# Optimization experiments

Hardware: AMD Instinct MI355X
Metric: run time of the kernel (lower is better)

The kernel has to match this reference:

```python
import jax, jax.numpy as jnp
import numpy as np
from jax import lax

B, C, H, W = 16, 128, 128, 128
WS, K = 2, 7
EPS = 1e-5


def setup_inputs() -> dict:
    key = jax.random.key(0)
    ks = jax.random.split(key, 4)
    s = 0.02
    return {
        "x": jax.random.normal(ks[0], (B, C, H, W), jnp.float32),
        "bn_gamma": jnp.ones((C,), jnp.float32),
        "bn_beta": jnp.zeros((C,), jnp.float32),
        "bn_mean": jnp.zeros((C,), jnp.float32),
        "bn_var": jnp.ones((C,), jnp.float32),
        "dw_w": jax.random.normal(ks[1], (C, 1, K, K), jnp.float32) * s,  # depthwise OIHW, groups=C
        "dw_b": jnp.zeros((C,), jnp.float32),
        "qkv_w": jax.random.normal(ks[2], (3 * C, C), jnp.float32) * s,  # 1x1 conv weight
        "qkv_b": jnp.zeros((3 * C,), jnp.float32),
        "proj_w": jax.random.normal(ks[3], (C, C), jnp.float32) * s,
        "proj_b": jnp.zeros((C,), jnp.float32),
    }


def reference(x, bn_gamma, bn_beta, bn_mean, bn_var, dw_w, dw_b, qkv_w, qkv_b, proj_w, proj_b):
    b, c, h, w = x.shape
    h2, w2 = h // WS, w // WS
    L = h2 * w2
    # --- ggm: BatchNorm (eval) -> GELU -> depthwise conv k=7 stride=2 pad=3 ---
    inv = lax.rsqrt(bn_var + EPS)
    xn = (x - bn_mean[None, :, None, None]) * (bn_gamma * inv)[None, :, None, None] + bn_beta[None, :, None, None]
    g = jax.nn.gelu(xn, approximate=False)
    guide = lax.conv_general_dilated(
        g, dw_w, window_strides=(WS, WS), padding=[(K // 2, K // 2), (K // 2, K // 2)],
        feature_group_count=c, dimension_numbers=("NCHW", "OIHW", "NCHW"),
    ) + dw_b[None, :, None, None]  # [B,C,H2,W2]
    # --- unfold(kernel=2, stride=2): non-overlapping 2x2 windows -> [B,C,4,L] ---
    xu = x.reshape(b, c, h2, WS, w2, WS).transpose(0, 1, 3, 5, 2, 4).reshape(b, c, WS * WS, L)
    tokens = jnp.concatenate([guide.reshape(b, c, 1, L), xu], axis=2)  # [B,C,5,L]
    # --- qkv 1x1 conv ---
    qkv = jnp.einsum("bcnl,dc->bdnl", tokens, qkv_w) + qkv_b[None, :, None, None]
    q, k, v = jnp.split(qkv, 3, axis=1)  # each [B,C,5,L]
    # --- tiny 5x5 attention per channel, contracting over the L window axis ---
    attn = jnp.einsum("bcnl,bcml->bcnm", q, k) / jnp.sqrt(jnp.float32(c))
    attn = jax.nn.softmax(attn, axis=-1)
    out = jnp.einsum("bcnm,bcml->bcnl", attn, v)  # [B,C,5,L]
    # take the guide-token row and fold back to the window grid
    out0 = out[:, :, 0, :].reshape(b, c, h2, w2)
    return jnp.einsum("bchw,dc->bdhw", out0, proj_w) + proj_b[None, :, None, None]
```

## Files before the change

### kernel.cpp

```cpp
#include <hip/hip_runtime.h>
#include <math.h>

#define BB 16
#define CC 128
#define HH 128
#define WW 128
#define LL 4096

typedef short short8 __attribute__((ext_vector_type(8)));
typedef float f32x4 __attribute__((ext_vector_type(4)));

__device__ __forceinline__ ushort f2bf(float f) {
    union { float f; unsigned u; } un; un.f = f;
    unsigned u = un.u;
    u += 0x7fffu + ((u >> 16) & 1u);
    return (ushort)(u >> 16);
}
__device__ __forceinline__ float bf2f(ushort h) {
    union { unsigned u; float f; } un; un.u = ((unsigned)h) << 16;
    return un.f;
}
__device__ __forceinline__ float fast_gelu(float xv) {
    float x2 = xv*xv;
    float arg = xv*(-2.3022100f - 0.1029436f*x2);
    float e = exp2f(arg);
    return xv*__builtin_amdgcn_rcpf(1.f + e);
}
__device__ __forceinline__ int swzkey(int r) { return (r & 3) ^ ((r >> 2) & 3); }

__global__ __launch_bounds__(128) void prep_cvec(
    const float* __restrict__ qkv_b, const float* __restrict__ proj_w,
    const float* __restrict__ proj_b, float* __restrict__ cvec)
{
    int t = threadIdx.x;
    float s = proj_b[t];
    const float* pr = proj_w + t*CC;
    const float* bv = qkv_b + 2*CC;
    for (int c = 0; c < CC; ++c) s += pr[c]*bv[c];
    cvec[t] = s;
}

__global__ __launch_bounds__(256) void guide_kernel(
    const float* __restrict__ x, const float* __restrict__ gamma,
    const float* __restrict__ beta, const float* __restrict__ mean,
    const float* __restrict__ var, const float* __restrict__ dww,
    const float* __restrict__ dwb, ushort* __restrict__ gw,
    float* __restrict__ Tpart)
{
    int bc = blockIdx.x;
    int b = bc >> 7, c = bc & 127;
    int ty = blockIdx.y;
    __shared__ __align__(16) float g[69*144];
    __shared__ float red[5][4];
    int t = threadIdx.x;
    int lane = t & 63, wave = t >> 6;
    float wreg[49];
    #pragma unroll
    for (int k = 0; k < 49; ++k) wreg[k] = dww[c*49 + k];
    float bias = dwb[c];
    float scl = gamma[c] * rsqrtf(var[c] + 1e-5f);
    float sft = beta[c] - mean[c]*scl;
    const float* xb = x + (size_t)(b*CC + c)*HH*WW;
    int ihbase = 64*ty - 3;
    float a00=0.f, a01=0.f, a10=0.f, a11=0.f;
    #pragma unroll
    for (int k = 0; k < 9; ++k) {
        int idx = k*256 + t;
        if (idx < 69*32) {
            int row = idx >> 5, ch = idx & 31;
            int ih = ihbase + row;
            float4 v4 = {0.f, 0.f, 0.f, 0.f};
            if ((unsigned)ih < 128u) {
                float4 xv = *(const float4*)(xb + ih*WW + 4*ch);
                if (row >= 3 && row < 67) {
                    float e0 = xv.x + xv.z, e1 = xv.y + xv.w;
                    if (ih & 1) { a10 += e0; a11 += e1; }
                    else        { a00 += e0; a01 += e1; }
                }
                v4.x = fast_gelu(xv.x*scl + sft);
                v4.y = fast_gelu(xv.y*scl + sft);
                v4.z = fast_gelu(xv.z*scl + sft);
                v4.w = fast_gelu(xv.w*scl + sft);
            }
            int f = (row >> 2) & 3;
            *(float4*)(g + row*144 + 4*((ch + 1) ^ f)) = v4;
        }
    }
    if (t < 138) {
        int row = t >> 1;
        int lc = (t & 1) ? 33 : 0;
        int f = (row >> 2) & 3;
        float4 z4 = {0.f, 0.f, 0.f, 0.f};
        *(float4*)(g + row*144 + 4*(lc ^ f)) = z4;
    }
    __syncthreads();
    int vg = t >> 4, owg = t & 15;
    float acc[2][4];
    #pragma unroll
    for (int v = 0; v < 2; ++v)
        #pragma unroll
        for (int hh = 0; hh < 4; ++hh) acc[v][hh] = bias;
    #pragma unroll
    for (int j = 0; j < 9; ++j) {
        int rr = 4*vg + j;
        int f = (rr >> 2) & 3;
        const float* grow = g + rr*144;
        float win[16];
        #pragma unroll
        for (int i = 0; i < 4; ++i) {
            float4 w4 = *(const float4*)(grow + 4*(((2*owg + i) ^ f)));
            win[4*i+0] = w4.x; win[4*i+1] = w4.y;
            win[4*i+2] = w4.z; win[4*i+3] = w4.w;
        }
        #pragma unroll
        for (int v = 0; v < 2; ++v) {
            int kh = j - 2*v;
            if (kh >= 0 && kh <= 6) {
                #pragma unroll
                for (int hh = 0; hh < 4; ++hh)
                    #pragma unroll
                    for (int kw = 0; kw < 7; ++kw)
                        acc[v][hh] += wreg[kh*7 + kw] * win[2*hh + kw + 1];
            }
        }
    }
    int orbase = 32*ty + 2*vg;
    ushort* gdst = gw + ((size_t)(b*CC + c) << 12);
    float gsum = 0.f;
    #pragma unroll
    for (int v = 0; v < 2; ++v) {
        uint2 pk;
        pk.x = (unsigned)f2bf(acc[v][0]) | ((unsigned)f2bf(acc[v][1]) << 16);
        pk.y = (unsigned)f2bf(acc[v][2]) | ((unsigned)f2bf(acc[v][3]) << 16);
        *(uint2*)(gdst + (orbase + v)*64 + 4*owg) = pk;
        gsum += acc[v][0] + acc[v][1] + acc[v][2] + acc[v][3];
    }
    float vals[5] = {gsum, a00, a01, a10, a11};
    #pragma unroll
    for (int v = 0; v < 5; ++v) {
        float s = vals[v];
        s += __shfl_xor(s, 1);  s += __shfl_xor(s, 2);
        s += __shfl_xor(s, 4);  s += __shfl_xor(s, 8);
        s += __shfl_xor(s, 16); s += __shfl_xor(s, 32);
        if (lane == 0) red[v][wave] = s;
    }
    __syncthreads();
    if (t < 5)
        Tpart[((size_t)(b*2 + ty)*5 + t)*128 + c] =
            red[t][0] + red[t][1] + red[t][2] + red[t][3];
}

__global__ __launch_bounds__(512) void gram_kernel(
    const float* __restrict__ x, const ushort* __restrict__ gw,
    float* __restrict__ Gpart)
{
    __shared__ __align__(16) ushort tokb[2*3*128*32];
    int t = threadIdx.x;
    int blk = blockIdx.x;
    int b = blk >> 4, kq = (blk >> 1) & 7, grp = blk & 1;
    int lane = t & 63, wid = t >> 6;
    int l15 = lane & 15, kg = lane >> 4;
    int js = t >> 2, sub = t & 3;
    int keyj = swzkey(js);
    const float* xrow0 = x + ((size_t)(b*CC + js)*HH + grp)*WW;
    const ushort* gwrow = gw + ((size_t)(b*CC + js) << 12);
    f32x4 acc[8][3];
    #pragma unroll
    for (int i = 0; i < 8; ++i)
        #pragma unroll
        for (int q = 0; q < 3; ++q) acc[i][q] = (f32x4){0.f,0.f,0.f,0.f};
    int H0 = kq*8;
    float4 xa, xbv, xc, xd;
    uint4 gr;
    {
        const float* xp = xrow0 + (2*H0)*WW + sub*16;
        xa = *(const float4*)(xp);
        xbv = *(const float4*)(xp + 4);
        xc = *(const float4*)(xp + 8);
        xd = *(const float4*)(xp + 12);
        gr = *(const uint4*)(gwrow + H0*64 + sub*8);
    }
    for (int s = 0; s < 16; ++s) {
        int cur = s & 1;
        ushort* tb = tokb + cur*(3*128*32);
        {
            unsigned lo0 = (unsigned)f2bf(xa.x) | ((unsigned)f2bf(xa.z) << 16);
            unsigned lo1 = (unsigned)f2bf(xbv.x) | ((unsigned)f2bf(xbv.z) << 16);
            unsigned lo2 = (unsigned)f2bf(xc.x) | ((unsigned)f2bf(xc.z) << 16);
            unsigned lo3 = (unsigned)f2bf(xd.x) | ((unsigned)f2bf(xd.z) << 16);
            unsigned hi0 = (unsigned)f2bf(xa.y) | ((unsigned)f2bf(xa.w) << 16);
            unsigned hi1 = (unsigned)f2bf(xbv.y) | ((unsigned)f2bf(xbv.w) << 16);
            unsigned hi2 = (unsigned)f2bf(xc.y) | ((unsigned)f2bf(xc.w) << 16);
            unsigned hi3 = (unsigned)f2bf(xd.y) | ((unsigned)f2bf(xd.w) << 16);
            uint4 lov = {lo0, lo1, lo2, lo3};
            uint4 hiv = {hi0, hi1, hi2, hi3};
            int chs = (sub ^ keyj) << 3;
            *(uint4*)(tb + (1*128 + js)*32 + chs) = lov;
            *(uint4*)(tb + (2*128 + js)*32 + chs) = hiv;
            *(uint4*)(tb + (0*128 + js)*32 + chs) = gr;
        }
        if (s < 15) {
            int sn = s + 1;
            int h = H0 + (sn >> 1), whalf = sn & 1;
            const float* xp = xrow0 + (2*h)*WW + whalf*64 + sub*16;
            xa = *(const float4*)(xp);
            xbv = *(const float4*)(xp + 4);
            xc = *(const float4*)(xp + 8);
            xd = *(const float4*)(xp + 12);
            gr = *(const uint4*)(gwrow + h*64 + whalf*32 + sub*8);
        }
        __syncthreads();
        const ushort* tb2 = tokb + cur*(3*128*32);
        short8 af[8];
        #pragma unroll
        for (int f = 0; f < 8; ++f) {
            int row = f*16 + l15;
            af[f] = *(const short8*)(tb2 + row*32 + ((kg ^ swzkey(row)) << 3));
        }
        if (grp == 0) {
            #pragma unroll
            for (int q = 0; q < 3; ++q) {
                int nf = wid*3 + q;
                int pl = nf >> 3, jr = (nf & 7)*16 + l15;
                short8 bf = *(const short8*)(tb2 + (pl*128 + jr)*32 + ((kg ^ swzkey(jr)) << 3));
                #pragma unroll
                for (int f = 0; f < 8; ++f)
                    acc[f][q] = __builtin_amdgcn_mfma_f32_16x16x32_bf16(af[f], bf, acc[f][q], 0, 0, 0);
            }
        } else {
            #pragma unroll
            for (int q = 0; q < 2; ++q) {
                int nf = wid*2 + q;
                int pl = 1 + (nf >> 3), jr = (nf & 7)*16 + l15;
                short8 bf = *(const short8*)(tb2 + (pl*128 + jr)*32 + ((kg ^ swzkey(jr)) << 3));
                #pragma unroll
                for (int f = 0; f < 8; ++f)
                    acc[f][q] = __builtin_amdgcn_mfma_f32_16x16x32_bf16(af[f], bf, acc[f][q], 0, 0, 0);
            }
        }
    }
    float* gp = Gpart + (size_t)(b*8 + kq)*81920;
    if (grp == 0) {
        #pragma unroll
        for (int f = 0; f < 8; ++f)
            #pragma unroll
            for (int q = 0; q < 3; ++q) {
                int n = (wid*3 + q)*16 + l15;
                #pragma unroll
                for (int r = 0; r < 4; ++r)
                    gp[(size_t)(f*16 + kg*4 + r)*640 + n] = acc[f][q][r];
            }
    } else {
        #pragma unroll
        for (int f = 0; f < 8; ++f)
            #pragma unroll
            for (int q = 0; q < 2; ++q) {
                int n = 384 + (wid*2 + q)*16 + l15;
                #pragma unroll
                for (int r = 0; r < 4; ++r)
                    gp[(size_t)(f*16 + kg*4 + r)*640 + n] = acc[f][q][r];
            }
    }
}

__global__ __launch_bounds__(256) void combine_kernel(
    const float* __restrict__ Gpart, const float* __restrict__ Tpart,
    const float* __restrict__ qkv_w, const float* __restrict__ qkv_b,
    float* __restrict__ Sout)
{
    __shared__ float Gm[128*129];
    __shared__ float Wks[128*129];
    __shared__ float Ts[5*128];
    int blk = blockIdx.x;
    int b = blk / 5, m = blk % 5;
    int t = threadIdx.x;
    for (int idx4 = t; idx4 < 4096; idx4 += 256) {
        int i = idx4 >> 5, j4 = idx4 & 31;
        float4 ws = {0.f,0.f,0.f,0.f};
        #pragma unroll
        for (int kq = 0; kq < 8; ++kq) {
            float4 v = *(const float4*)(Gpart + (size_t)(b*8+kq)*81920
                                        + (size_t)i*640 + m*128 + j4*4);
            ws.x += v.x; ws.y += v.y; ws.z += v.z; ws.w += v.w;
        }
        Gm[i*129 + j4*4 + 0] = ws.x;
        Gm[i*129 + j4*4 + 1] = ws.y;
        Gm[i*129 + j4*4 + 2] = ws.z;
        Gm[i*129 + j4*4 + 3] = ws.w;
        float4 wk = *(const float4*)(qkv_w + (size_t)(128 + i)*128 + j4*4);
        Wks[i*129 + j4*4 + 0] = wk.x;
        Wks[i*129 + j4*4 + 1] = wk.y;
        Wks[i*129 + j4*4 + 2] = wk.z;
        Wks[i*129 + j4*4 + 3] = wk.w;
    }
    for (int i2 = t; i2 < 640; i2 += 256) {
        int v = i2 >> 7, c = i2 & 127;
        Ts[v*128 + c] = Tpart[((size_t)(b*2 + 0)*5 + v)*128 + c]
                      + Tpart[((size_t)(b*2 + 1)*5 + v)*128 + c];
    }
    __syncthreads();
    int ti = t >> 4, tc = t & 15;
    float au[8][8];
    #pragma unroll
    for (int r = 0; r < 8; ++r)
        #pragma unroll
        for (int s2 = 0; s2 < 8; ++s2) au[r][s2] = 0.f;
    for (int j = 0; j < 128; ++j) {
        float gmr[8], wkr[8];
        #pragma unroll
        for (int r = 0; r < 8; ++r) gmr[r] = Gm[(ti*8 + r)*129 + j];
        #pragma unroll
        for (int s2 = 0; s2 < 8; ++s2) wkr[s2] = Wks[(tc*8 + s2)*129 + j];
        #pragma unroll
        for (int r = 0; r < 8; ++r)
            #pragma unroll
            for (int s2 = 0; s2 < 8; ++s2) au[r][s2] += gmr[r]*wkr[s2];
    }
    __syncthreads();
    #pragma unroll
    for (int r = 0; r < 8; ++r)
        #pragma unroll
        for (int s2 = 0; s2 < 8; ++s2)
            Gm[(ti*8 + r)*129 + tc*8 + s2] = au[r][s2];
    __syncthreads();
    if (t < 128) {
        int c = t;
        const float4* wq4p = (const float4*)(qkv_w + (size_t)c*128);
        float bq = qkv_b[c], bk = qkv_b[128 + c];
        float ud = 0.f, t0d = 0.f, km = 0.f;
        for (int k4 = 0; k4 < 32; ++k4) {
            float4 w4 = wq4p[k4];
            int k = k4*4;
            ud  += w4.x*Gm[(k+0)*129 + c] + w4.y*Gm[(k+1)*129 + c]
                 + w4.z*Gm[(k+2)*129 + c] + w4.w*Gm[(k+3)*129 + c];
            t0d += w4.x*Ts[k+0] + w4.y*Ts[k+1] + w4.z*Ts[k+2] + w4.w*Ts[k+3];
            km  += Wks[c*129 + k+0]*Ts[m*128 + k+0] + Wks[c*129 + k+1]*Ts[m*128 + k+1]
                 + Wks[c*129 + k+2]*Ts[m*128 + k+2] + Wks[c*129 + k+3]*Ts[m*128 + k+3];
        }
        Sout[(size_t)(b*128 + c)*5 + m] = ud + bq*km + bk*t0d + 4096.0f*bq*bk;
    }
}

__global__ __launch_bounds__(128) void softmax_attn(
    const float* __restrict__ Sout, float* __restrict__ attn)
{
    int b = blockIdx.x, c = threadIdx.x;
    const float* sp = Sout + (size_t)(b*128 + c)*5;
    const float scale = 0.08838834764831845f;
    float s[5];
    #pragma unroll
    for (int m = 0; m < 5; ++m) s[m] = sp[m]*scale;
    float mx = s[0];
    #pragma unroll
    for (int m = 1; m < 5; ++m) mx = fmaxf(mx, s[m]);
    float e[5], tot = 0.f;
    #pragma unroll
    for (int m = 0; m < 5; ++m) { e[m] = expf(s[m] - mx); tot += e[m]; }
    float inv = 1.f/tot;
    #pragma unroll
    for (int m = 0; m < 5; ++m) attn[(size_t)(b*128 + c)*5 + m] = e[m]*inv;
}

__global__ __launch_bounds__(256) void pw_kernel(
    const float* __restrict__ qkv_w, const float* __restrict__ proj_w,
    const float* __restrict__ attn, ushort* __restrict__ PW)
{
    __shared__ float attns[CC];
    __shared__ float wvs[32*CC];
    int blk = blockIdx.x;
    int b = blk / 5, m = blk % 5;
    int t = threadIdx.x;
    if (t < CC) attns[t] = attn[(b*CC + t)*5 + m];
    int d = t >> 1, cb = (t & 1)*64;
    float acc[64];
    #pragma unroll
    for (int j = 0; j < 64; ++j) acc[j] = 0.f;
    for (int cc0 = 0; cc0 < CC; cc0 += 32) {
        __syncthreads();
        for (int idx = t; idx < 32*CC; idx += 256) {
            int row = idx >> 7, col = idx & 127;
            wvs[idx] = qkv_w[(2*CC + cc0 + row)*CC + col];
        }
        __syncthreads();
        for (int cl = 0; cl < 32; ++cl) {
            int c = cc0 + cl;
            float a = proj_w[d*CC + c]*attns[c];
            const float* wr = wvs + cl*CC + cb;
            #pragma unroll
            for (int j = 0; j < 64; ++j) acc[j] += a*wr[j];
        }
    }
    ushort* dst = PW + ((size_t)(b*5 + m) << 14) + d*CC + cb;
    #pragma unroll
    for (int j = 0; j < 64; ++j) dst[j] = f2bf(acc[j]);
}

__device__ __forceinline__ void stage_chunk(
    ushort* __restrict__ tok, float* __restrict__ xt,
    const float* __restrict__ x, const ushort* __restrict__ gw,
    int b, int h, int whalf, int t)
{
    {
        int c = t >> 1, r = t & 1;
        const ushort* gsrc = gw + ((size_t)(b*CC + c) << 12) + h*64 + whalf*32 + r*16;
        uint4 g0 = *(const uint4*)gsrc;
        uint4 g1 = *(const uint4*)(gsrc + 8);
        unsigned wd[8] = {g0.x,g0.y,g0.z,g0.w,g1.x,g1.y,g1.z,g1.w};
        #pragma unroll
        for (int k2 = 0; k2 < 8; ++k2) {
            int lp0 = r*16 + 2*k2, lp1 = lp0 + 1;
            tok[lp0*128 + (c ^ ((lp0 & 7) << 3))] = (ushort)wd[k2];
            tok[lp1*128 + (c ^ ((lp1 & 7) << 3))] = (ushort)(wd[k2] >> 16);
        }
    }
    int cp = t & 15, lgrp = t >> 4;
    for (int slab = 0; slab < 4; ++slab) {
        int c0 = slab*32;
        __syncthreads();
        #pragma unroll
        for (int i = 0; i < 4; ++i) {
            int fc = i*256 + t;
            int cc = fc >> 5, f4 = fc & 31;
            int r = f4 >> 4, wq = f4 & 15;
            float4 v = *(const float4*)(x + ((size_t)(b*CC + c0 + cc)*HH + 2*h + r)*WW
                                          + whalf*64 + 4*wq);
            *(float4*)(xt + cc*132 + f4*4) = v;
        }
        __syncthreads();
        #pragma unroll
        for (int sub = 0; sub < 2; ++sub) {
            int lp = lgrp*2 + sub;
            int key8 = (lp & 7) << 3;
            int slot = ((c0 + 2*cp) ^ key8) >> 1;
            #pragma unroll
            for (int r = 0; r < 2; ++r) {
                float2 lo = *(const float2*)(xt + (2*cp    )*132 + r*64 + 2*lp);
                float2 hi = *(const float2*)(xt + (2*cp + 1)*132 + r*64 + 2*lp);
                unsigned w0 = (unsigned)f2bf(lo.x) | ((unsigned)f2bf(hi.x) << 16);
                unsigned w1 = (unsigned)f2bf(lo.y) | ((unsigned)f2bf(hi.y) << 16);
                ((unsigned*)(tok + (1 + 2*r)*4096 + lp*128))[slot] = w0;
                ((unsigned*)(tok + (2 + 2*r)*4096 + lp*128))[slot] = w1;
            }
        }
    }
    __syncthreads();
}

__global__ __launch_bounds__(256) void y_kernel(
    const float* __restrict__ x, const ushort* __restrict__ gw,
    const ushort* __restrict__ PW, const float* __restrict__ cvec,
    float* __restrict__ out)
{
    __shared__ __align__(16) ushort tok[5*32*128];
    __shared__ __align__(16) float xt[32*132];
    int t = threadIdx.x;
    int blk = blockIdx.x;
    int b = blk >> 7, chunk = blk & 127;
    int h = chunk >> 1, whalf = chunk & 1;
    int lane = t & 63, wave = t >> 6;
    int l15 = lane & 15, kg = lane >> 4;
    int swz = (l15 & 7) << 3;
    stage_chunk(tok, xt, x, gw, b, h, whalf, t);
    f32x4 acc[2][2] = {};
    #pragma unroll
    for (int m = 0; m < 5; ++m) {
        const ushort* pwb = PW + ((size_t)(b*5 + m) << 14)
                          + ((wave*32 + l15) << 7) + (kg << 3);
        #pragma unroll
        for (int kt = 0; kt < 4; ++kt) {
            int ko = (kt*32 + kg*8) ^ swz;
            short8 a0 = *(const short8*)(tok + m*4096 + (l15     )*128 + ko);
            short8 a1 = *(const short8*)(tok + m*4096 + (16 + l15)*128 + ko);
            short8 b0 = *(const short8*)(pwb + kt*32);
            short8 b1 = *(const short8*)(pwb + (16 << 7) + kt*32);
            acc[0][0] = __builtin_amdgcn_mfma_f32_16x16x32_bf16(a0, b0, acc[0][0], 0, 0, 0);
            acc[0][1] = __builtin_amdgcn_mfma_f32_16x16x32_bf16(a0, b1, acc[0][1], 0, 0, 0);
            acc[1][0] = __builtin_amdgcn_mfma_f32_16x16x32_bf16(a1, b0, acc[1][0], 0, 0, 0);
            acc[1][1] = __builtin_amdgcn_mfma_f32_16x16x32_bf16(a1, b1, acc[1][1], 0, 0, 0);
        }
    }
    __syncthreads();
    float* ylds = (float*)tok;
    #pragma unroll
    for (int mt = 0; mt < 2; ++mt)
        #pragma unroll
        for (int ntl = 0; ntl < 2; ++ntl) {
            int cc = wave*32 + ntl*16 + l15;
            float cv = cvec[cc];
            #pragma unroll
            for (int rr = 0; rr < 4; ++rr) {
                int l = mt*16 + kg*4 + rr;
                ylds[cc*36 + l] = acc[mt][ntl][rr] + cv;
            }
        }
    __syncthreads();
    int c = t >> 1, half = t & 1;
    float* ob = out + ((size_t)(b*CC + c) << 12) + h*64 + whalf*32 + half*16;
    const float* yr = ylds + c*36 + half*16;
    #pragma unroll
    for (int j = 0; j < 4; ++j)
        ((float4*)ob)[j] = ((const float4*)yr)[j];
}

extern "C" void kernel_launch(void* const* d_in, const int* in_sizes, int n_in,
                              void* d_out, int out_size, void* d_ws, size_t ws_size,
                              hipStream_t stream) {
    const float* x        = (const float*)d_in[0];
    const float* bn_gamma = (const float*)d_in[1];
    const float* bn_beta  = (const float*)d_in[2];
    const float* bn_mean  = (const float*)d_in[3];
    const float* bn_var   = (const float*)d_in[4];
    const float* dw_w     = (const float*)d_in[5];
    const float* dw_b     = (const float*)d_in[6];
    const float* qkv_w    = (const float*)d_in[7];
    const float* qkv_b    = (const float*)d_in[8];
    const float* proj_w   = (const float*)d_in[9];
    const float* proj_b   = (const float*)d_in[10];
    float* out = (float*)d_out;

    char* w = (char*)d_ws;
    ushort* gw    = (ushort*)w; w += (size_t)BB*CC*LL*2;
    ushort* PW    = (ushort*)w; w += (size_t)BB*5*CC*CC*2;
    float*  Gpart = (float*)w;  w += (size_t)16*8*128*640*4;
    float*  Tpart = (float*)w;  w += (size_t)BB*2*5*128*4;
    float*  Sout  = (float*)w;  w += (size_t)BB*CC*5*4;
    float*  attn  = (float*)w;  w += (size_t)BB*CC*5*4;
    float*  cvec  = (float*)w;  w += (size_t)CC*4;

    prep_cvec<<<1, 128, 0, stream>>>(qkv_b, proj_w, proj_b, cvec);
    guide_kernel<<<dim3(BB*CC, 2), 256, 0, stream>>>(
        x, bn_gamma, bn_beta, bn_mean, bn_var, dw_w, dw_b, gw, Tpart);
    gram_kernel<<<256, 512, 0, stream>>>(x, gw, Gpart);
    combine_kernel<<<80, 256, 0, stream>>>(Gpart, Tpart, qkv_w, qkv_b, Sout);
    softmax_attn<<<BB, 128, 0, stream>>>(Sout, attn);
    pw_kernel<<<BB*5, 256, 0, stream>>>(qkv_w, proj_w, attn, PW);
    y_kernel<<<2048, 256, 0, stream>>>(x, gw, PW, cvec, out);
}
```

Measured before the change: 240.1 us.

## Pre-transpose x into bf16 token layout and feed y_kernel MFMA from global

Adds an xperm kernel that converts x to bf16 in a [B,4,L,C] token-major layout and also computes the per-window token sums. y_kernel then loads its A operands straight from this buffer instead of staging and transposing fp32 x through LDS. Token-sum reductions move out of guide_kernel into gram and xperm, and gram splits H into 16 chunks for more blocks. This adds an extra full pass over x plus a 64MB intermediate write, and doubles the Gram partial traffic that combine must sum.

```diff
diff --git a/kernel.cpp b/kernel.cpp
--- a/kernel.cpp
+++ b/kernel.cpp
@@ -44,16 +44,13 @@
     const float* __restrict__ x, const float* __restrict__ gamma,
     const float* __restrict__ beta, const float* __restrict__ mean,
     const float* __restrict__ var, const float* __restrict__ dww,
-    const float* __restrict__ dwb, ushort* __restrict__ gw,
-    float* __restrict__ Tpart)
+    const float* __restrict__ dwb, ushort* __restrict__ gw)
 {
     int bc = blockIdx.x;
     int b = bc >> 7, c = bc & 127;
     int ty = blockIdx.y;
     __shared__ __align__(16) float g[69*144];
-    __shared__ float red[5][4];
-    int t = threadIdx.x;
-    int lane = t & 63, wave = t >> 6;
+    int t = threadIdx.x;
     float wreg[49];
     #pragma unroll
     for (int k = 0; k < 49; ++k) wreg[k] = dww[c*49 + k];
@@ -62,7 +59,6 @@
     float sft = beta[c] - mean[c]*scl;
     const float* xb = x + (size_t)(b*CC + c)*HH*WW;
     int ihbase = 64*ty - 3;
-    float a00=0.f, a01=0.f, a10=0.f, a11=0.f;
     #pragma unroll
     for (int k = 0; k < 9; ++k) {
         int idx = k*256 + t;
@@ -72,11 +68,6 @@
             float4 v4 = {0.f, 0.f, 0.f, 0.f};
             if ((unsigned)ih < 128u) {
                 float4 xv = *(const float4*)(xb + ih*WW + 4*ch);
-                if (row >= 3 && row < 67) {
-                    float e0 = xv.x + xv.z, e1 = xv.y + xv.w;
-                    if (ih & 1) { a10 += e0; a11 += e1; }
-                    else        { a00 += e0; a01 += e1; }
-                }
                 v4.x = fast_gelu(xv.x*scl + sft);
                 v4.y = fast_gelu(xv.y*scl + sft);
                 v4.z = fast_gelu(xv.z*scl + sft);
@@ -126,38 +117,78 @@
     }
     int orbase = 32*ty + 2*vg;
     ushort* gdst = gw + ((size_t)(b*CC + c) << 12);
-    float gsum = 0.f;
     #pragma unroll
     for (int v = 0; v < 2; ++v) {
         uint2 pk;
         pk.x = (unsigned)f2bf(acc[v][0]) | ((unsigned)f2bf(acc[v][1]) << 16);
         pk.y = (unsigned)f2bf(acc[v][2]) | ((unsigned)f2bf(acc[v][3]) << 16);
         *(uint2*)(gdst + (orbase + v)*64 + 4*owg) = pk;
-        gsum += acc[v][0] + acc[v][1] + acc[v][2] + acc[v][3];
-    }
-    float vals[5] = {gsum, a00, a01, a10, a11};
-    #pragma unroll
-    for (int v = 0; v < 5; ++v) {
-        float s = vals[v];
-        s += __shfl_xor(s, 1);  s += __shfl_xor(s, 2);
-        s += __shfl_xor(s, 4);  s += __shfl_xor(s, 8);
-        s += __shfl_xor(s, 16); s += __shfl_xor(s, 32);
-        if (lane == 0) red[v][wave] = s;
-    }
-    __syncthreads();
-    if (t < 5)
-        Tpart[((size_t)(b*2 + ty)*5 + t)*128 + c] =
-            red[t][0] + red[t][1] + red[t][2] + red[t][3];
+    }
+}
+
+__global__ __launch_bounds__(256) void xperm_kernel(
+    const float* __restrict__ x, ushort* __restrict__ xu, float* __restrict__ Txp)
+{
+    __shared__ __align__(16) float xs[32*130];
+    int b = blockIdx.x, hg = blockIdx.y;
+    int t = threadIdx.x;
+    int c_l = t >> 3, wq = t & 7;
+    int ww = t >> 1, chalf = t & 1;
+    float pacc[4][4];
+    #pragma unroll
+    for (int i = 0; i < 4; ++i)
+        #pragma unroll
+        for (int j = 0; j < 4; ++j) pacc[i][j] = 0.f;
+    #pragma unroll
+    for (int hh2 = 0; hh2 < 2; ++hh2) {
+        int hh = hg*2 + hh2;
+        #pragma unroll
+        for (int cs = 0; cs < 4; ++cs) {
+            __syncthreads();
+            const float* xp = x + ((size_t)(b*CC + cs*32 + c_l)*HH + hh)*WW + wq*16;
+            #pragma unroll
+            for (int i = 0; i < 4; ++i) {
+                float4 v = *(const float4*)(xp + i*4);
+                *(float4*)(xs + c_l*130 + wq*16 + i*4) = v;
+                pacc[cs][hh2*2 + 0] += v.x + v.z;
+                pacc[cs][hh2*2 + 1] += v.y + v.w;
+            }
+            __syncthreads();
+            float vals[16];
+            #pragma unroll
+            for (int j = 0; j < 16; ++j) vals[j] = xs[(chalf*16 + j)*130 + ww];
+            unsigned pk[8];
+            #pragma unroll
+            for (int k = 0; k < 8; ++k)
+                pk[k] = (unsigned)f2bf(vals[2*k]) | ((unsigned)f2bf(vals[2*k+1]) << 16);
+            int m = hh2*2 + (ww & 1);
+            int l = hg*64 + (ww >> 1);
+            ushort* dst = xu + ((size_t)(b*4 + m)*LL + l)*CC + cs*32 + chalf*16;
+            uint4 o0 = {pk[0], pk[1], pk[2], pk[3]};
+            uint4 o1 = {pk[4], pk[5], pk[6], pk[7]};
+            *(uint4*)dst = o0;
+            *(uint4*)(dst + 8) = o1;
+        }
+    }
+    #pragma unroll
+    for (int cs = 0; cs < 4; ++cs)
+        #pragma unroll
+        for (int mm = 0; mm < 4; ++mm) {
+            float v = pacc[cs][mm];
+            v += __shfl_xor(v, 1); v += __shfl_xor(v, 2); v += __shfl_xor(v, 4);
+            if (wq == 0)
+                Txp[((size_t)(b*64 + hg)*4 + mm)*128 + cs*32 + c_l] = v;
+        }
 }
 
 __global__ __launch_bounds__(512) void gram_kernel(
     const float* __restrict__ x, const ushort* __restrict__ gw,
-    float* __restrict__ Gpart)
+    float* __restrict__ Gpart, float* __restrict__ Tg)
 {
     __shared__ __align__(16) ushort tokb[2*3*128*32];
     int t = threadIdx.x;
     int blk = blockIdx.x;
-    int b = blk >> 4, kq = (blk >> 1) & 7, grp = blk & 1;
+    int b = blk >> 5, kq = (blk >> 1) & 15, grp = blk & 1;
     int lane = t & 63, wid = t >> 6;
     int l15 = lane & 15, kg = lane >> 4;
     int js = t >> 2, sub = t & 3;
@@ -169,7 +200,8 @@
     for (int i = 0; i < 8; ++i)
         #pragma unroll
         for (int q = 0; q < 3; ++q) acc[i][q] = (f32x4){0.f,0.f,0.f,0.f};
-    int H0 = kq*8;
+    float tacc = 0.f;
+    int H0 = kq*4;
     float4 xa, xbv, xc, xd;
     uint4 gr;
     {
@@ -180,9 +212,15 @@
         xd = *(const float4*)(xp + 12);
         gr = *(const uint4*)(gwrow + H0*64 + sub*8);
     }
-    for (int s = 0; s < 16; ++s) {
+    for (int s = 0; s < 8; ++s) {
         int cur = s & 1;
         ushort* tb = tokb + cur*(3*128*32);
+        if (grp == 0) {
+            tacc += bf2f((ushort)gr.x) + bf2f((ushort)(gr.x >> 16))
+                  + bf2f((ushort)gr.y) + bf2f((ushort)(gr.y >> 16))
+                  + bf2f((ushort)gr.z) + bf2f((ushort)(gr.z >> 16))
+                  + bf2f((ushort)gr.w) + bf2f((ushort)(gr.w >> 16));
+        }
         {
             unsigned lo0 = (unsigned)f2bf(xa.x) | ((unsigned)f2bf(xa.z) << 16);
             unsigned lo1 = (unsigned)f2bf(xbv.x) | ((unsigned)f2bf(xbv.z) << 16);
@@ -199,7 +237,7 @@
             *(uint4*)(tb + (2*128 + js)*32 + chs) = hiv;
             *(uint4*)(tb + (0*128 + js)*32 + chs) = gr;
         }
-        if (s < 15) {
+        if (s < 7) {
             int sn = s + 1;
             int h = H0 + (sn >> 1), whalf = sn & 1;
             const float* xp = xrow0 + (2*h)*WW + whalf*64 + sub*16;
@@ -239,7 +277,11 @@
             }
         }
     }
-    float* gp = Gpart + (size_t)(b*8 + kq)*81920;
+    if (grp == 0) {
+        tacc += __shfl_xor(tacc, 1); tacc += __shfl_xor(tacc, 2);
+        if (sub == 0) Tg[(size_t)(b*16 + kq)*128 + js] = tacc;
+    }
+    float* gp = Gpart + (size_t)(b*16 + kq)*81920;
     if (grp == 0) {
         #pragma unroll
         for (int f = 0; f < 8; ++f)
@@ -264,9 +306,9 @@
 }
 
 __global__ __launch_bounds__(256) void combine_kernel(
-    const float* __restrict__ Gpart, const float* __restrict__ Tpart,
-    const float* __restrict__ qkv_w, const float* __restrict__ qkv_b,
-    float* __restrict__ Sout)
+    const float* __restrict__ Gpart, const float* __restrict__ Tg,
+    const float* __restrict__ Txp, const float* __restrict__ qkv_w,
+    const float* __restrict__ qkv_b, float* __restrict__ Sout)
 {
     __shared__ float Gm[128*129];
     __shared__ float Wks[128*129];
@@ -278,8 +320,8 @@
         int i = idx4 >> 5, j4 = idx4 & 31;
         float4 ws = {0.f,0.f,0.f,0.f};
         #pragma unroll
-        for (int kq = 0; kq < 8; ++kq) {
-            float4 v = *(const float4*)(Gpart + (size_t)(b*8+kq)*81920
+        for (int kq = 0; kq < 16; ++kq) {
+            float4 v = *(const float4*)(Gpart + (size_t)(b*16+kq)*81920
                                         + (size_t)i*640 + m*128 + j4*4);
             ws.x += v.x; ws.y += v.y; ws.z += v.z; ws.w += v.w;
         }
@@ -295,8 +337,14 @@
     }
     for (int i2 = t; i2 < 640; i2 += 256) {
         int v = i2 >> 7, c = i2 & 127;
-        Ts[v*128 + c] = Tpart[((size_t)(b*2 + 0)*5 + v)*128 + c]
-                      + Tpart[((size_t)(b*2 + 1)*5 + v)*128 + c];
+        float s = 0.f;
+        if (v == 0) {
+            for (int p = 0; p < 16; ++p) s += Tg[(size_t)(b*16 + p)*128 + c];
+        } else {
+            for (int p = 0; p < 64; ++p)
+                s += Txp[((size_t)(b*64 + p)*4 + (v - 1))*128 + c];
+        }
+        Ts[v*128 + c] = s;
     }
     __syncthreads();
     int ti = t >> 4, tc = t & 15;
@@ -395,11 +443,20 @@
     for (int j = 0; j < 64; ++j) dst[j] = f2bf(acc[j]);
 }
 
-__device__ __forceinline__ void stage_chunk(
-    ushort* __restrict__ tok, float* __restrict__ xt,
-    const float* __restrict__ x, const ushort* __restrict__ gw,
-    int b, int h, int whalf, int t)
-{
+__global__ __launch_bounds__(256) void y_kernel(
+    const ushort* __restrict__ xu, const ushort* __restrict__ gw,
+    const ushort* __restrict__ PW, const float* __restrict__ cvec,
+    float* __restrict__ out)
+{
+    __shared__ __align__(16) ushort tok0[32*128];
+    __shared__ __align__(16) float ylds[128*36];
+    int t = threadIdx.x;
+    int blk = blockIdx.x;
+    int b = blk >> 7, chunk = blk & 127;
+    int h = chunk >> 1, whalf = chunk & 1;
+    int lane = t & 63, wave = t >> 6;
+    int l15 = lane & 15, kg = lane >> 4;
+    int swz = (l15 & 7) << 3;
     {
         int c = t >> 1, r = t & 1;
         const ushort* gsrc = gw + ((size_t)(b*CC + c) << 12) + h*64 + whalf*32 + r*16;
@@ -409,68 +466,33 @@
         #pragma unroll
         for (int k2 = 0; k2 < 8; ++k2) {
             int lp0 = r*16 + 2*k2, lp1 = lp0 + 1;
-            tok[lp0*128 + (c ^ ((lp0 & 7) << 3))] = (ushort)wd[k2];
-            tok[lp1*128 + (c ^ ((lp1 & 7) << 3))] = (ushort)(wd[k2] >> 16);
-        }
-    }
-    int cp = t & 15, lgrp = t >> 4;
-    for (int slab = 0; slab < 4; ++slab) {
-        int c0 = slab*32;
-        __syncthreads();
-        #pragma unroll
-        for (int i = 0; i < 4; ++i) {
-            int fc = i*256 + t;
-            int cc = fc >> 5, f4 = fc & 31;
-            int r = f4 >> 4, wq = f4 & 15;
-            float4 v = *(const float4*)(x + ((size_t)(b*CC + c0 + cc)*HH + 2*h + r)*WW
-                                          + whalf*64 + 4*wq);
-            *(float4*)(xt + cc*132 + f4*4) = v;
-        }
-        __syncthreads();
-        #pragma unroll
-        for (int sub = 0; sub < 2; ++sub) {
-            int lp = lgrp*2 + sub;
-            int key8 = (lp & 7) << 3;
-            int slot = ((c0 + 2*cp) ^ key8) >> 1;
-            #pragma unroll
-            for (int r = 0; r < 2; ++r) {
-                float2 lo = *(const float2*)(xt + (2*cp    )*132 + r*64 + 2*lp);
-                float2 hi = *(const float2*)(xt + (2*cp + 1)*132 + r*64 + 2*lp);
-                unsigned w0 = (unsigned)f2bf(lo.x) | ((unsigned)f2bf(hi.x) << 16);
-                unsigned w1 = (unsigned)f2bf(lo.y) | ((unsigned)f2bf(hi.y) << 16);
-                ((unsigned*)(tok + (1 + 2*r)*4096 + lp*128))[slot] = w0;
-                ((unsigned*)(tok + (2 + 2*r)*4096 + lp*128))[slot] = w1;
-            }
+            tok0[lp0*128 + (c ^ ((lp0 & 7) << 3))] = (ushort)wd[k2];
+            tok0[lp1*128 + (c ^ ((lp1 & 7) << 3))] = (ushort)(wd[k2] >> 16);
         }
     }
     __syncthreads();
-}
-
-__global__ __launch_bounds__(256) void y_kernel(
-    const float* __restrict__ x, const ushort* __restrict__ gw,
-    const ushort* __restrict__ PW, const float* __restrict__ cvec,
-    float* __restrict__ out)
-{
-    __shared__ __align__(16) ushort tok[5*32*128];
-    __shared__ __align__(16) float xt[32*132];
-    int t = threadIdx.x;
-    int blk = blockIdx.x;
-    int b = blk >> 7, chunk = blk & 127;
-    int h = chunk >> 1, whalf = chunk & 1;
-    int lane = t & 63, wave = t >> 6;
-    int l15 = lane & 15, kg = lane >> 4;
-    int swz = (l15 & 7) << 3;
-    stage_chunk(tok, xt, x, gw, b, h, whalf, t);
     f32x4 acc[2][2] = {};
-    #pragma unroll
-    for (int m = 0; m < 5; ++m) {
-        const ushort* pwb = PW + ((size_t)(b*5 + m) << 14)
-                          + ((wave*32 + l15) << 7) + (kg << 3);
+    const ushort* pwb0 = PW + ((size_t)(b*5) << 14) + ((wave*32 + l15) << 7) + (kg << 3);
+    #pragma unroll
+    for (int kt = 0; kt < 4; ++kt) {
+        int ko = (kt*32 + kg*8) ^ swz;
+        short8 a0 = *(const short8*)(tok0 + (l15     )*128 + ko);
+        short8 a1 = *(const short8*)(tok0 + (16 + l15)*128 + ko);
+        short8 b0 = *(const short8*)(pwb0 + kt*32);
+        short8 b1 = *(const short8*)(pwb0 + (16 << 7) + kt*32);
+        acc[0][0] = __builtin_amdgcn_mfma_f32_16x16x32_bf16(a0, b0, acc[0][0], 0, 0, 0);
+        acc[0][1] = __builtin_amdgcn_mfma_f32_16x16x32_bf16(a0, b1, acc[0][1], 0, 0, 0);
+        acc[1][0] = __builtin_amdgcn_mfma_f32_16x16x32_bf16(a1, b0, acc[1][0], 0, 0, 0);
+        acc[1][1] = __builtin_amdgcn_mfma_f32_16x16x32_bf16(a1, b1, acc[1][1], 0, 0, 0);
+    }
+    #pragma unroll
+    for (int mt = 1; mt <= 4; ++mt) {
+        const ushort* ab = xu + ((size_t)(b*4 + mt - 1)*LL + h*64 + whalf*32)*CC;
+        const ushort* pwb = pwb0 + ((size_t)mt << 14);
         #pragma unroll
         for (int kt = 0; kt < 4; ++kt) {
-            int ko = (kt*32 + kg*8) ^ swz;
-            short8 a0 = *(const short8*)(tok + m*4096 + (l15     )*128 + ko);
-            short8 a1 = *(const short8*)(tok + m*4096 + (16 + l15)*128 + ko);
+            short8 a0 = *(const short8*)(ab + (l15     )*CC + kt*32 + kg*8);
+            short8 a1 = *(const short8*)(ab + (16 + l15)*CC + kt*32 + kg*8);
             short8 b0 = *(const short8*)(pwb + kt*32);
             short8 b1 = *(const short8*)(pwb + (16 << 7) + kt*32);
             acc[0][0] = __builtin_amdgcn_mfma_f32_16x16x32_bf16(a0, b0, acc[0][0], 0, 0, 0);
@@ -479,18 +501,16 @@
             acc[1][1] = __builtin_amdgcn_mfma_f32_16x16x32_bf16(a1, b1, acc[1][1], 0, 0, 0);
         }
     }
-    __syncthreads();
-    float* ylds = (float*)tok;
-    #pragma unroll
-    for (int mt = 0; mt < 2; ++mt)
+    #pragma unroll
+    for (int mt2 = 0; mt2 < 2; ++mt2)
         #pragma unroll
         for (int ntl = 0; ntl < 2; ++ntl) {
             int cc = wave*32 + ntl*16 + l15;
             float cv = cvec[cc];
             #pragma unroll
             for (int rr = 0; rr < 4; ++rr) {
-                int l = mt*16 + kg*4 + rr;
-                ylds[cc*36 + l] = acc[mt][ntl][rr] + cv;
+                int l = mt2*16 + kg*4 + rr;
+                ylds[cc*36 + l] = acc[mt2][ntl][rr] + cv;
             }
         }
     __syncthreads();
@@ -520,19 +540,22 @@
 
     char* w = (char*)d_ws;
     ushort* gw    = (ushort*)w; w += (size_t)BB*CC*LL*2;
+    ushort* xu    = (ushort*)w; w += (size_t)BB*4*LL*CC*2;
     ushort* PW    = (ushort*)w; w += (size_t)BB*5*CC*CC*2;
-    float*  Gpart = (float*)w;  w += (size_t)16*8*128*640*4;
-    float*  Tpart = (float*)w;  w += (size_t)BB*2*5*128*4;
+    float*  Gpart = (float*)w;  w += (size_t)BB*16*81920*4;
+    float*  Tg    = (float*)w;  w += (size_t)BB*16*128*4;
+    float*  Txp   = (float*)w;  w += (size_t)BB*64*4*128*4;
     float*  Sout  = (float*)w;  w += (size_t)BB*CC*5*4;
     float*  attn  = (float*)w;  w += (size_t)BB*CC*5*4;
     float*  cvec  = (float*)w;  w += (size_t)CC*4;
 
     prep_cvec<<<1, 128, 0, stream>>>(qkv_b, proj_w, proj_b, cvec);
     guide_kernel<<<dim3(BB*CC, 2), 256, 0, stream>>>(
-        x, bn_gamma, bn_beta, bn_mean, bn_var, dw_w, dw_b, gw, Tpart);
-    gram_kernel<<<256, 512, 0, stream>>>(x, gw, Gpart);
-    combine_kernel<<<80, 256, 0, stream>>>(Gpart, Tpart, qkv_w, qkv_b, Sout);
+        x, bn_gamma, bn_beta, bn_mean, bn_var, dw_w, dw_b, gw);
+    xperm_kernel<<<dim3(BB, 64), 256, 0, stream>>>(x, xu, Txp);
+    gram_kernel<<<512, 512, 0, stream>>>(x, gw, Gpart, Tg);
+    combine_kernel<<<80, 256, 0, stream>>>(Gpart, Tg, Txp, qkv_w, qkv_b, Sout);
     softmax_attn<<<BB, 128, 0, stream>>>(Sout, attn);
     pw_kernel<<<BB*5, 256, 0, stream>>>(qkv_w, proj_w, attn, PW);
-    y_kernel<<<2048, 256, 0, stream>>>(x, gw, PW, cvec, out);
-}
+    y_kernel<<<2048, 256, 0, stream>>>(xu, gw, PW, cvec, out);
+}
```

Result: slower. 323.4 us (+34.7%).

## Split gram kernel K-range finer and move token sums into gram kernel

Applied to the files above, without the earlier changes.

The gram kernel grid doubles from 256 to 512 blocks, with each block covering 4 rows of H instead of 8, so more blocks can be resident across the GPU's compute units. The per-channel token sums (guide and the four unfold positions) move out of guide_kernel, which loses its reductions and extra syncthreads, and are accumulated in gram_kernel from values already in registers. The cost is a Gpart buffer twice as large that combine_kernel must read and reduce over 16 partials instead of 8, plus a small strided reduction for the token sums.

```diff
diff --git a/kernel.cpp b/kernel.cpp
--- a/kernel.cpp
+++ b/kernel.cpp
@@ -44,16 +44,13 @@
     const float* __restrict__ x, const float* __restrict__ gamma,
     const float* __restrict__ beta, const float* __restrict__ mean,
     const float* __restrict__ var, const float* __restrict__ dww,
-    const float* __restrict__ dwb, ushort* __restrict__ gw,
-    float* __restrict__ Tpart)
+    const float* __restrict__ dwb, ushort* __restrict__ gw)
 {
     int bc = blockIdx.x;
     int b = bc >> 7, c = bc & 127;
     int ty = blockIdx.y;
     __shared__ __align__(16) float g[69*144];
-    __shared__ float red[5][4];
     int t = threadIdx.x;
-    int lane = t & 63, wave = t >> 6;
     float wreg[49];
     #pragma unroll
     for (int k = 0; k < 49; ++k) wreg[k] = dww[c*49 + k];
@@ -62,7 +59,6 @@
     float sft = beta[c] - mean[c]*scl;
     const float* xb = x + (size_t)(b*CC + c)*HH*WW;
     int ihbase = 64*ty - 3;
-    float a00=0.f, a01=0.f, a10=0.f, a11=0.f;
     #pragma unroll
     for (int k = 0; k < 9; ++k) {
         int idx = k*256 + t;
@@ -72,11 +68,6 @@
             float4 v4 = {0.f, 0.f, 0.f, 0.f};
             if ((unsigned)ih < 128u) {
                 float4 xv = *(const float4*)(xb + ih*WW + 4*ch);
-                if (row >= 3 && row < 67) {
-                    float e0 = xv.x + xv.z, e1 = xv.y + xv.w;
-                    if (ih & 1) { a10 += e0; a11 += e1; }
-                    else        { a00 += e0; a01 += e1; }
-                }
                 v4.x = fast_gelu(xv.x*scl + sft);
                 v4.y = fast_gelu(xv.y*scl + sft);
                 v4.z = fast_gelu(xv.z*scl + sft);
@@ -126,38 +117,23 @@
     }
     int orbase = 32*ty + 2*vg;
     ushort* gdst = gw + ((size_t)(b*CC + c) << 12);
-    float gsum = 0.f;
     #pragma unroll
     for (int v = 0; v < 2; ++v) {
         uint2 pk;
         pk.x = (unsigned)f2bf(acc[v][0]) | ((unsigned)f2bf(acc[v][1]) << 16);
         pk.y = (unsigned)f2bf(acc[v][2]) | ((unsigned)f2bf(acc[v][3]) << 16);
         *(uint2*)(gdst + (orbase + v)*64 + 4*owg) = pk;
-        gsum += acc[v][0] + acc[v][1] + acc[v][2] + acc[v][3];
-    }
-    float vals[5] = {gsum, a00, a01, a10, a11};
-    #pragma unroll
-    for (int v = 0; v < 5; ++v) {
-        float s = vals[v];
-        s += __shfl_xor(s, 1);  s += __shfl_xor(s, 2);
-        s += __shfl_xor(s, 4);  s += __shfl_xor(s, 8);
-        s += __shfl_xor(s, 16); s += __shfl_xor(s, 32);
-        if (lane == 0) red[v][wave] = s;
-    }
-    __syncthreads();
-    if (t < 5)
-        Tpart[((size_t)(b*2 + ty)*5 + t)*128 + c] =
-            red[t][0] + red[t][1] + red[t][2] + red[t][3];
+    }
 }
 
 __global__ __launch_bounds__(512) void gram_kernel(
     const float* __restrict__ x, const ushort* __restrict__ gw,
-    float* __restrict__ Gpart)
+    float* __restrict__ Gpart, float* __restrict__ Tg, float* __restrict__ Txg)
 {
     __shared__ __align__(16) ushort tokb[2*3*128*32];
     int t = threadIdx.x;
     int blk = blockIdx.x;
-    int b = blk >> 4, kq = (blk >> 1) & 7, grp = blk & 1;
+    int b = blk >> 5, kq = (blk >> 1) & 15, grp = blk & 1;
     int lane = t & 63, wid = t >> 6;
     int l15 = lane & 15, kg = lane >> 4;
     int js = t >> 2, sub = t & 3;
@@ -169,7 +145,8 @@
     for (int i = 0; i < 8; ++i)
         #pragma unroll
         for (int q = 0; q < 3; ++q) acc[i][q] = (f32x4){0.f,0.f,0.f,0.f};
-    int H0 = kq*8;
+    float tacc = 0.f, ps0 = 0.f, ps1 = 0.f;
+    int H0 = kq*4;
     float4 xa, xbv, xc, xd;
     uint4 gr;
     {
@@ -180,9 +157,17 @@
         xd = *(const float4*)(xp + 12);
         gr = *(const uint4*)(gwrow + H0*64 + sub*8);
     }
-    for (int s = 0; s < 16; ++s) {
+    for (int s = 0; s < 8; ++s) {
         int cur = s & 1;
         ushort* tb = tokb + cur*(3*128*32);
+        if (grp == 0) {
+            tacc += bf2f((ushort)gr.x) + bf2f((ushort)(gr.x >> 16))
+                  + bf2f((ushort)gr.y) + bf2f((ushort)(gr.y >> 16))
+                  + bf2f((ushort)gr.z) + bf2f((ushort)(gr.z >> 16))
+                  + bf2f((ushort)gr.w) + bf2f((ushort)(gr.w >> 16));
+        }
+        ps0 += xa.x + xa.z + xbv.x + xbv.z + xc.x + xc.z + xd.x + xd.z;
+        ps1 += xa.y + xa.w + xbv.y + xbv.w + xc.y + xc.w + xd.y + xd.w;
         {
             unsigned lo0 = (unsigned)f2bf(xa.x) | ((unsigned)f2bf(xa.z) << 16);
             unsigned lo1 = (unsigned)f2bf(xbv.x) | ((unsigned)f2bf(xbv.z) << 16);
@@ -199,7 +184,7 @@
             *(uint4*)(tb + (2*128 + js)*32 + chs) = hiv;
             *(uint4*)(tb + (0*128 + js)*32 + chs) = gr;
         }
-        if (s < 15) {
+        if (s < 7) {
             int sn = s + 1;
             int h = H0 + (sn >> 1), whalf = sn & 1;
             const float* xp = xrow0 + (2*h)*WW + whalf*64 + sub*16;
@@ -239,7 +224,18 @@
             }
         }
     }
-    float* gp = Gpart + (size_t)(b*8 + kq)*81920;
+    ps0 += __shfl_xor(ps0, 1); ps0 += __shfl_xor(ps0, 2);
+    ps1 += __shfl_xor(ps1, 1); ps1 += __shfl_xor(ps1, 2);
+    if (grp == 0) {
+        tacc += __shfl_xor(tacc, 1); tacc += __shfl_xor(tacc, 2);
+        if (sub == 0) Tg[(size_t)(b*16 + kq)*128 + js] = tacc;
+    }
+    if (sub == 0) {
+        float* tx = Txg + (((size_t)(b*16 + kq)*2 + grp)*2)*128;
+        tx[js] = ps0;
+        tx[128 + js] = ps1;
+    }
+    float* gp = Gpart + (size_t)(b*16 + kq)*81920;
     if (grp == 0) {
         #pragma unroll
         for (int f = 0; f < 8; ++f)
@@ -264,9 +260,9 @@
 }
 
 __global__ __launch_bounds__(256) void combine_kernel(
-    const float* __restrict__ Gpart, const float* __restrict__ Tpart,
-    const float* __restrict__ qkv_w, const float* __restrict__ qkv_b,
-    float* __restrict__ Sout)
+    const float* __restrict__ Gpart, const float* __restrict__ Tg,
+    const float* __restrict__ Txg, const float* __restrict__ qkv_w,
+    const float* __restrict__ qkv_b, float* __restrict__ Sout)
 {
     __shared__ float Gm[128*129];
     __shared__ float Wks[128*129];
@@ -278,8 +274,8 @@
         int i = idx4 >> 5, j4 = idx4 & 31;
         float4 ws = {0.f,0.f,0.f,0.f};
         #pragma unroll
-        for (int kq = 0; kq < 8; ++kq) {
-            float4 v = *(const float4*)(Gpart + (size_t)(b*8+kq)*81920
+        for (int kq = 0; kq < 16; ++kq) {
+            float4 v = *(const float4*)(Gpart + (size_t)(b*16+kq)*81920
                                         + (size_t)i*640 + m*128 + j4*4);
             ws.x += v.x; ws.y += v.y; ws.z += v.z; ws.w += v.w;
         }
@@ -295,8 +291,15 @@
     }
     for (int i2 = t; i2 < 640; i2 += 256) {
         int v = i2 >> 7, c = i2 & 127;
-        Ts[v*128 + c] = Tpart[((size_t)(b*2 + 0)*5 + v)*128 + c]
-                      + Tpart[((size_t)(b*2 + 1)*5 + v)*128 + c];
+        float s = 0.f;
+        if (v == 0) {
+            for (int p = 0; p < 16; ++p) s += Tg[(size_t)(b*16 + p)*128 + c];
+        } else {
+            int grp = (v - 1) >> 1, pi = (v - 1) & 1;
+            for (int p = 0; p < 16; ++p)
+                s += Txg[(((size_t)(b*16 + p)*2 + grp)*2 + pi)*128 + c];
+        }
+        Ts[v*128 + c] = s;
     }
     __syncthreads();
     int ti = t >> 4, tc = t & 15;
@@ -521,17 +524,18 @@
     char* w = (char*)d_ws;
     ushort* gw    = (ushort*)w; w += (size_t)BB*CC*LL*2;
     ushort* PW    = (ushort*)w; w += (size_t)BB*5*CC*CC*2;
-    float*  Gpart = (float*)w;  w += (size_t)16*8*128*640*4;
-    float*  Tpart = (float*)w;  w += (size_t)BB*2*5*128*4;
+    float*  Gpart = (float*)w;  w += (size_t)BB*16*81920*4;
+    float*  Tg    = (float*)w;  w += (size_t)BB*16*128*4;
+    float*  Txg   = (float*)w;  w += (size_t)BB*16*2*2*128*4;
     float*  Sout  = (float*)w;  w += (size_t)BB*CC*5*4;
     float*  attn  = (float*)w;  w += (size_t)BB*CC*5*4;
     float*  cvec  = (float*)w;  w += (size_t)CC*4;
 
     prep_cvec<<<1, 128, 0, stream>>>(qkv_b, proj_w, proj_b, cvec);
     guide_kernel<<<dim3(BB*CC, 2), 256, 0, stream>>>(
-        x, bn_gamma, bn_beta, bn_mean, bn_var, dw_w, dw_b, gw, Tpart);
-    gram_kernel<<<256, 512, 0, stream>>>(x, gw, Gpart);
-    combine_kernel<<<80, 256, 0, stream>>>(Gpart, Tpart, qkv_w, qkv_b, Sout);
+        x, bn_gamma, bn_beta, bn_mean, bn_var, dw_w, dw_b, gw);
+    gram_kernel<<<512, 512, 0, stream>>>(x, gw, Gpart, Tg, Txg);
+    combine_kernel<<<80, 256, 0, stream>>>(Gpart, Tg, Txg, qkv_w, qkv_b, Sout);
     softmax_attn<<<BB, 128, 0, stream>>>(Sout, attn);
     pw_kernel<<<BB*5, 256, 0, stream>>>(qkv_w, proj_w, attn, PW);
     y_kernel<<<2048, 256, 0, stream>>>(x, gw, PW, cvec, out);
```

Measured after the change: 245.9 us. 1.02x slower.
